# Optimization experiments

Hardware: AMD Instinct MI355X
Metric: run time of the kernel (lower is better)

## Reference

```python
import jax, jax.numpy as jnp
import numpy as np

B, S, D, H = 2, 2048, 1024, 16
Dh = D // H
LN_EPS = 1e-5


def setup_inputs() -> dict:
    key = jax.random.key(0)
    ks = jax.random.split(key, 14)
    s = 1.0 / np.sqrt(D)
    return {
        "q": jax.random.normal(ks[0], (B, S, D), jnp.float32),
        "k": jax.random.normal(ks[1], (B, S, D), jnp.float32),
        "v": jax.random.normal(ks[2], (B, S, D), jnp.float32),
        "attn_mask": jax.random.randint(ks[3], (B, S, S), 0, 2).astype(bool),
        "Wq": jax.random.normal(ks[4], (D, D), jnp.float32) * s,
        "bq": jnp.zeros((D,), jnp.float32),
        "Wk": jax.random.normal(ks[5], (D, D), jnp.float32) * s,
        "bk": jnp.zeros((D,), jnp.float32),
        "Wv": jax.random.normal(ks[6], (D, D), jnp.float32) * s,
        "bv": jnp.zeros((D,), jnp.float32),
        "Wo": jax.random.normal(ks[7], (D, D), jnp.float32) * s,
        "bo": jnp.zeros((D,), jnp.float32),
        "gamma": jnp.ones((D,), jnp.float32),
        "beta": jnp.zeros((D,), jnp.float32),
    }


def reference(q, k, v, attn_mask, Wq, bq, Wk, bk, Wv, bv, Wo, bo, gamma, beta):
    residual = q
    # projections (W stored as [in, out])
    qh = (q @ Wq + bq).reshape(B, S, H, Dh).transpose(0, 2, 1, 3)  # [B,H,S,Dh]
    kh = (k @ Wk + bk).reshape(B, S, H, Dh).transpose(0, 2, 1, 3)
    vh = (v @ Wv + bv).reshape(B, S, H, Dh).transpose(0, 2, 1, 3)
    scores = jnp.einsum("bhqd,bhkd->bhqk", qh, kh) / np.sqrt(Dh)
    scores = jnp.where(attn_mask[:, None, :, :], -1e9, scores)
    attn = jax.nn.softmax(scores, axis=-1)  # dropout is identity in eval
    context = jnp.einsum("bhqk,bhkd->bhqd", attn, vh)  # [B,H,S,Dh]
    # faithful to original bug: flat reshape WITHOUT transposing heads back
    context = context.reshape(B, S, D)
    out = context @ Wo + bo
    x = residual + out
    mu = jnp.mean(x, axis=-1, keepdims=True)
    var = jnp.var(x, axis=-1, keepdims=True)
    out = (x - mu) / jnp.sqrt(var + LN_EPS) * gamma + beta
    return out, attn
```

## Files before the change

### kernel.cpp

```cpp
#include <hip/hip_runtime.h>
#include <hip/hip_bf16.h>

typedef __attribute__((ext_vector_type(8))) short bf16x8;
typedef __attribute__((ext_vector_type(4))) float f32x4;

__device__ __forceinline__ short f2bf(float f) {
    union { float f; unsigned u; } v; v.f = f;
    unsigned r = (v.u + 0x7FFFu + ((v.u >> 16) & 1u)) >> 16;
    return (short)r;
}
__device__ __forceinline__ float bf2f(short s) {
    union { unsigned u; float f; } v; v.u = ((unsigned)(unsigned short)s) << 16;
    return v.f;
}
__device__ __forceinline__ void gll16(const void* g, void* l) {
    __builtin_amdgcn_global_load_lds(
        (const __attribute__((address_space(1))) unsigned int*)g,
        (__attribute__((address_space(3))) unsigned int*)l, 16, 0, 0);
}

#define QSCALE 0.18033688011112042f

__global__ __launch_bounds__(256) void k_prep(
    const float* __restrict__ qin, const float* __restrict__ kin, const float* __restrict__ vin,
    short* __restrict__ qbf, short* __restrict__ kbf, short* __restrict__ vbf,
    const float* __restrict__ Wq, const float* __restrict__ Wk,
    const float* __restrict__ Wv, const float* __restrict__ Wo,
    short* __restrict__ WqT, short* __restrict__ WkT,
    short* __restrict__ WvT, short* __restrict__ WoT,
    const int* __restrict__ mask, unsigned* __restrict__ mb)
{
    __shared__ int sm[8192];
    const int bid = blockIdx.x, tid = threadIdx.x;
    if (bid < 6144) {
        const float* in = bid < 2048 ? qin : (bid < 4096 ? kin : vin);
        short* out = bid < 2048 ? qbf : (bid < 4096 ? kbf : vbf);
        const long i = ((long)(bid & 2047) * 256 + tid) * 8;
        float4 f0 = *reinterpret_cast<const float4*>(&in[i]);
        float4 f1 = *reinterpret_cast<const float4*>(&in[i + 4]);
        bf16x8 v;
        v[0] = f2bf(f0.x); v[1] = f2bf(f0.y); v[2] = f2bf(f0.z); v[3] = f2bf(f0.w);
        v[4] = f2bf(f1.x); v[5] = f2bf(f1.y); v[6] = f2bf(f1.z); v[7] = f2bf(f1.w);
        *reinterpret_cast<bf16x8*>(&out[i]) = v;
    } else if (bid < 10240) {
        const int t2 = bid - 6144, which = t2 >> 10, local = t2 & 1023;
        const float* W = which == 0 ? Wq : (which == 1 ? Wk : (which == 2 ? Wv : Wo));
        short* WT = which == 0 ? WqT : (which == 1 ? WkT : (which == 2 ? WvT : WoT));
        float (*t)[33] = reinterpret_cast<float(*)[33]>(sm);
        const int rb = (local >> 5) * 32, cb = (local & 31) * 32;
        const int tr = tid >> 3, tc = (tid & 7) * 4;
        const float4 v = *reinterpret_cast<const float4*>(&W[(long)(rb + tr) * 1024 + cb + tc]);
        t[tr][tc + 0] = v.x; t[tr][tc + 1] = v.y; t[tr][tc + 2] = v.z; t[tr][tc + 3] = v.w;
        __syncthreads();
        short4 o;
        o.x = f2bf(t[tc + 0][tr]); o.y = f2bf(t[tc + 1][tr]);
        o.z = f2bf(t[tc + 2][tr]); o.w = f2bf(t[tc + 3][tr]);
        *reinterpret_cast<short4*>(&WT[(long)(cb + tr) * 1024 + rb + tc]) = o;
    } else {
        const long base = (long)(bid - 10240) * 8192;
#pragma unroll
        for (int i = 0; i < 8; ++i)
            *reinterpret_cast<int4*>(&sm[i * 1024 + tid * 4]) =
                *reinterpret_cast<const int4*>(&mask[base + i * 1024 + tid * 4]);
        __syncthreads();
        unsigned wv = 0;
#pragma unroll
        for (int j = 0; j < 32; ++j) wv |= (sm[tid * 32 + j] != 0 ? 1u : 0u) << j;
        mb[base / 32 + tid] = wv;
    }
}

__global__ __launch_bounds__(256) void k_gemm_qkv(
    const short* __restrict__ A0, const short* __restrict__ A1, const short* __restrict__ A2,
    const short* __restrict__ B0, const short* __restrict__ B1, const short* __restrict__ B2,
    const float* __restrict__ b0, const float* __restrict__ b1, const float* __restrict__ b2,
    short* __restrict__ o0, short* __restrict__ o1, short* __restrict__ o2)
{
    __shared__ short As[128 * 64];
    __shared__ short Bs[128 * 64];
    const int z = blockIdx.z;
    const short* A = z == 0 ? A0 : (z == 1 ? A1 : A2);
    const short* BT = z == 0 ? B0 : (z == 1 ? B1 : B2);
    const float* bias = z == 0 ? b0 : (z == 1 ? b1 : b2);
    short* outp = z == 0 ? o0 : (z == 1 ? o1 : o2);
    const float scale = z == 0 ? QSCALE : 1.0f;

    const int tid = threadIdx.x, w = tid >> 6, lane = tid & 63;
    const int lr = lane & 15, lg = lane >> 4;
    const int rowbase = blockIdx.y * 128, colbase = blockIdx.x * 128;
    const int wr = (w >> 1) * 64, wc = (w & 1) * 64;
    const int srow = lane >> 3, sc_ = (lane & 7) ^ srow;

    f32x4 acc[4][4] = {};

    for (int kb = 0; kb < 1024; kb += 64) {
#pragma unroll
        for (int ii = 0; ii < 4; ++ii) {
            const int rl = w * 32 + ii * 8 + srow;
            gll16(A + (long)(rowbase + rl) * 1024 + kb + sc_ * 8, &As[(w * 32 + ii * 8) * 64]);
            gll16(BT + (long)(colbase + rl) * 1024 + kb + sc_ * 8, &Bs[(w * 32 + ii * 8) * 64]);
        }
        __syncthreads();
#pragma unroll
        for (int ks = 0; ks < 2; ++ks) {
            bf16x8 a[4], bq[4];
#pragma unroll
            for (int m = 0; m < 4; ++m) {
                const int r = wr + m * 16 + lr;
                a[m] = *reinterpret_cast<const bf16x8*>(&As[r * 64 + (((ks * 4 + lg) ^ (r & 7)) << 3)]);
            }
#pragma unroll
            for (int n = 0; n < 4; ++n) {
                const int r = wc + n * 16 + lr;
                bq[n] = *reinterpret_cast<const bf16x8*>(&Bs[r * 64 + (((ks * 4 + lg) ^ (r & 7)) << 3)]);
            }
#pragma unroll
            for (int m = 0; m < 4; ++m)
#pragma unroll
                for (int n = 0; n < 4; ++n)
                    acc[m][n] = __builtin_amdgcn_mfma_f32_16x16x32_bf16(a[m], bq[n], acc[m][n], 0, 0, 0);
        }
        __syncthreads();
    }

#pragma unroll
    for (int m = 0; m < 4; ++m) {
#pragma unroll
        for (int n = 0; n < 4; ++n) {
            const int C = colbase + wc + n * 16 + lr;
            const float bv = bias[C];
#pragma unroll
            for (int rr = 0; rr < 4; ++rr) {
                const int R = rowbase + wr + m * 16 + lg * 4 + rr;
                const float val = (acc[m][n][rr] + bv) * scale;
                const int b = R >> 11, s = R & 2047, h = C >> 6, dh = C & 63;
                if (z != 2)
                    outp[(((long)(b * 16 + h) * 2048 + s) << 6) + dh] = f2bf(val);
                else
                    outp[(((long)(b * 16 + h) * 64 + dh) << 11) + s] = f2bf(val);
            }
        }
    }
}

__global__ __launch_bounds__(256) void k_gemm_o(
    const short* __restrict__ A, const short* __restrict__ BT,
    const float* __restrict__ bias, const float* __restrict__ resid,
    float* __restrict__ outp)
{
    __shared__ short As[128 * 64];
    __shared__ short Bs[128 * 64];
    const int tid = threadIdx.x, w = tid >> 6, lane = tid & 63;
    const int lr = lane & 15, lg = lane >> 4;
    const int rowbase = blockIdx.y * 128, colbase = blockIdx.x * 128;
    const int wr = (w >> 1) * 64, wc = (w & 1) * 64;
    const int srow = lane >> 3, sc_ = (lane & 7) ^ srow;

    f32x4 acc[4][4] = {};

    for (int kb = 0; kb < 1024; kb += 64) {
#pragma unroll
        for (int ii = 0; ii < 4; ++ii) {
            const int rl = w * 32 + ii * 8 + srow;
            gll16(A + (long)(rowbase + rl) * 1024 + kb + sc_ * 8, &As[(w * 32 + ii * 8) * 64]);
            gll16(BT + (long)(colbase + rl) * 1024 + kb + sc_ * 8, &Bs[(w * 32 + ii * 8) * 64]);
        }
        __syncthreads();
#pragma unroll
        for (int ks = 0; ks < 2; ++ks) {
            bf16x8 a[4], bq[4];
#pragma unroll
            for (int m = 0; m < 4; ++m) {
                const int r = wr + m * 16 + lr;
                a[m] = *reinterpret_cast<const bf16x8*>(&As[r * 64 + (((ks * 4 + lg) ^ (r & 7)) << 3)]);
            }
#pragma unroll
            for (int n = 0; n < 4; ++n) {
                const int r = wc + n * 16 + lr;
                bq[n] = *reinterpret_cast<const bf16x8*>(&Bs[r * 64 + (((ks * 4 + lg) ^ (r & 7)) << 3)]);
            }
#pragma unroll
            for (int m = 0; m < 4; ++m)
#pragma unroll
                for (int n = 0; n < 4; ++n)
                    acc[m][n] = __builtin_amdgcn_mfma_f32_16x16x32_bf16(a[m], bq[n], acc[m][n], 0, 0, 0);
        }
        __syncthreads();
    }

#pragma unroll
    for (int m = 0; m < 4; ++m) {
#pragma unroll
        for (int n = 0; n < 4; ++n) {
            const int C = colbase + wc + n * 16 + lr;
            const float bv = bias[C];
#pragma unroll
            for (int rr = 0; rr < 4; ++rr) {
                const int R = rowbase + wr + m * 16 + lg * 4 + rr;
                const long idx = (long)R * 1024 + C;
                outp[idx] = acc[m][n][rr] + bv + resid[idx];
            }
        }
    }
}

__global__ __launch_bounds__(256, 4) void k_attn(
    const short* __restrict__ qh, const short* __restrict__ kh,
    const short* __restrict__ vt, const unsigned* __restrict__ mbits,
    float* __restrict__ attn_out, short* __restrict__ ctxb)
{
    const int g = blockIdx.x, xcd = g & 7, u = g >> 3;
    const int bh = u >> 2, qt = xcd * 4 + (u & 3);
    const int b = bh >> 4;
    const int tid = threadIdx.x, w = tid >> 6, lane = tid & 63;
    const int lr = lane & 15, lg = lane >> 4;
    const int irow = qt * 64 + w * 16;
    const long arow = (long)bh * 2048 + irow;

    __shared__ short Ks[2][64 * 64];
    __shared__ short Vs[2][64 * 64];
    __shared__ short Ps[4][16 * 64];

    const short* qhp = qh + arow * 64;
    const short* khp = kh + (long)bh * 131072;
    const short* vtp = vt + (long)bh * 131072;
    const unsigned* mbp = mbits + (long)b * 131072 + (long)irow * 64;

    const bf16x8 aq0 = *reinterpret_cast<const bf16x8*>(&qhp[lr * 64 + lg * 8]);
    const bf16x8 aq1 = *reinterpret_cast<const bf16x8*>(&qhp[lr * 64 + 32 + lg * 8]);
    const int srow = lane >> 3, sc_ = (lane & 7) ^ srow;

    auto stage_k = [&](int buf, int ch) {
#pragma unroll
        for (int ii = 0; ii < 2; ++ii) {
            const int r0 = w * 16 + ii * 8;
            gll16(khp + (long)(ch * 64 + r0 + srow) * 64 + sc_ * 8, &Ks[buf][r0 * 64]);
        }
    };
    auto stage_v = [&](int buf, int ch) {
#pragma unroll
        for (int ii = 0; ii < 2; ++ii) {
            const int r0 = w * 16 + ii * 8;
            gll16(vtp + (long)(r0 + srow) * 2048 + ch * 64 + sc_ * 8, &Vs[buf][r0 * 64]);
        }
    };
    auto kfrag = [&](int buf, int t, int ks) -> bf16x8 {
        const int r = t * 16 + lr;
        return *reinterpret_cast<const bf16x8*>(&Ks[buf][r * 64 + (((ks * 4 + lg) ^ (r & 7)) << 3)]);
    };
    auto vfrag = [&](int buf, int gi, int ks) -> bf16x8 {
        const int r = gi * 16 + lr;
        return *reinterpret_cast<const bf16x8*>(&Vs[buf][r * 64 + (((ks * 4 + lg) ^ (r & 7)) << 3)]);
    };
    auto ps_write = [&](int row, int t, float p) {
        const int ch8 = (t * 2 + (lr >> 3)) ^ (row & 7);
        Ps[w][row * 64 + (ch8 << 3) + (lr & 7)] = f2bf(p);
    };

    float l[4] = {0.f, 0.f, 0.f, 0.f};
    f32x4 acc[4] = {};

    stage_k(0, 0); stage_v(0, 0);
    asm volatile("s_waitcnt vmcnt(0)" ::: "memory");
    __builtin_amdgcn_s_barrier();
    asm volatile("" ::: "memory");

    for (int ch = 0; ch < 32; ++ch) {
        const int cur = ch & 1;
        unsigned mw[4][2];
#pragma unroll
        for (int rr = 0; rr < 4; ++rr) {
            mw[rr][0] = mbp[(lg * 4 + rr) * 64 + ch * 2];
            mw[rr][1] = mbp[(lg * 4 + rr) * 64 + ch * 2 + 1];
        }
        asm volatile("" ::: "memory");
        if (ch < 31) { stage_k(cur ^ 1, ch + 1); stage_v(cur ^ 1, ch + 1); }
        asm volatile("" ::: "memory");

#pragma unroll
        for (int t = 0; t < 4; ++t) {
            f32x4 sc = {};
            sc = __builtin_amdgcn_mfma_f32_16x16x32_bf16(aq0, kfrag(cur, t, 0), sc, 0, 0, 0);
            sc = __builtin_amdgcn_mfma_f32_16x16x32_bf16(aq1, kfrag(cur, t, 1), sc, 0, 0, 0);
#pragma unroll
            for (int rr = 0; rr < 4; ++rr) {
                const bool masked = (mw[rr][t >> 1] >> (((t & 1) << 4) + lr)) & 1;
                const float p = exp2f(masked ? -1e9f : sc[rr]);
                l[rr] += p;
                ps_write(lg * 4 + rr, t, p);
            }
        }
        const bf16x8 pa0 = *reinterpret_cast<const bf16x8*>(&Ps[w][lr * 64 + (((0 * 4 + lg) ^ (lr & 7)) << 3)]);
        const bf16x8 pa1 = *reinterpret_cast<const bf16x8*>(&Ps[w][lr * 64 + (((1 * 4 + lg) ^ (lr & 7)) << 3)]);
#pragma unroll
        for (int gi = 0; gi < 4; ++gi) {
            acc[gi] = __builtin_amdgcn_mfma_f32_16x16x32_bf16(pa0, vfrag(cur, gi, 0), acc[gi], 0, 0, 0);
            acc[gi] = __builtin_amdgcn_mfma_f32_16x16x32_bf16(pa1, vfrag(cur, gi, 1), acc[gi], 0, 0, 0);
        }
        asm volatile("s_waitcnt vmcnt(0)" ::: "memory");
        __builtin_amdgcn_s_barrier();
        asm volatile("" ::: "memory");
    }

    float C[4];
#pragma unroll
    for (int rr = 0; rr < 4; ++rr) {
#pragma unroll
        for (int off = 1; off < 16; off <<= 1) l[rr] += __shfl_xor(l[rr], off, 16);
        l[rr] = fmaxf(l[rr], 1e-30f);
        C[rr] = log2f(l[rr]);
    }
#pragma unroll
    for (int gi = 0; gi < 4; ++gi)
#pragma unroll
        for (int rr = 0; rr < 4; ++rr)
            ctxb[(arow + lg * 4 + rr) * 64 + gi * 16 + lr] = f2bf(acc[gi][rr] / l[rr]);

    stage_k(0, 0);
    asm volatile("s_waitcnt vmcnt(0)" ::: "memory");
    __builtin_amdgcn_s_barrier();
    asm volatile("" ::: "memory");

    for (int ch = 0; ch < 32; ++ch) {
        const int cur = ch & 1;
        unsigned mw[4][2];
#pragma unroll
        for (int rr = 0; rr < 4; ++rr) {
            mw[rr][0] = mbp[(lg * 4 + rr) * 64 + ch * 2];
            mw[rr][1] = mbp[(lg * 4 + rr) * 64 + ch * 2 + 1];
        }
        asm volatile("" ::: "memory");
        if (ch < 31) stage_k(cur ^ 1, ch + 1);
        asm volatile("" ::: "memory");

#pragma unroll
        for (int t = 0; t < 4; ++t) {
            f32x4 sc = {};
            sc = __builtin_amdgcn_mfma_f32_16x16x32_bf16(aq0, kfrag(cur, t, 0), sc, 0, 0, 0);
            sc = __builtin_amdgcn_mfma_f32_16x16x32_bf16(aq1, kfrag(cur, t, 1), sc, 0, 0, 0);
#pragma unroll
            for (int rr = 0; rr < 4; ++rr) {
                const bool masked = (mw[rr][t >> 1] >> (((t & 1) << 4) + lr)) & 1;
                const float p = exp2f((masked ? -1e9f : sc[rr]) - C[rr]);
                ps_write(lg * 4 + rr, t, p);
            }
        }
#pragma unroll
        for (int i2 = 0; i2 < 4; ++i2) {
            const int r = i2 * 4 + lg;
            const short4 p4 = *reinterpret_cast<const short4*>(
                &Ps[w][r * 64 + ((((lr >> 1)) ^ (r & 7)) << 3) + ((lr & 1) << 2)]);
            float4 o;
            o.x = bf2f(p4.x); o.y = bf2f(p4.y); o.z = bf2f(p4.z); o.w = bf2f(p4.w);
            *reinterpret_cast<float4*>(&attn_out[(arow + r) * 2048 + ch * 64 + lr * 4]) = o;
        }
        asm volatile("s_waitcnt vmcnt(4)" ::: "memory");
        __builtin_amdgcn_s_barrier();
        asm volatile("" ::: "memory");
    }
}

__global__ __launch_bounds__(256) void k_ln(const float* __restrict__ x,
    const float* __restrict__ gamma, const float* __restrict__ beta,
    float* __restrict__ out)
{
    __shared__ float red[8];
    const int r = blockIdx.x, tid = threadIdx.x;
    const float4 v = reinterpret_cast<const float4*>(x + (long)r * 1024)[tid];
    float s = v.x + v.y + v.z + v.w;
    float q2 = v.x * v.x + v.y * v.y + v.z * v.z + v.w * v.w;
#pragma unroll
    for (int off = 32; off; off >>= 1) {
        s += __shfl_xor(s, off, 64);
        q2 += __shfl_xor(q2, off, 64);
    }
    if ((tid & 63) == 0) { red[(tid >> 6) * 2] = s; red[(tid >> 6) * 2 + 1] = q2; }
    __syncthreads();
    s = red[0] + red[2] + red[4] + red[6];
    q2 = red[1] + red[3] + red[5] + red[7];
    const float mu = s * (1.0f / 1024.0f);
    const float var = q2 * (1.0f / 1024.0f) - mu * mu;
    const float rs = rsqrtf(var + 1e-5f);
    const float4 gm = reinterpret_cast<const float4*>(gamma)[tid];
    const float4 bb = reinterpret_cast<const float4*>(beta)[tid];
    float4 o;
    o.x = (v.x - mu) * rs * gm.x + bb.x;
    o.y = (v.y - mu) * rs * gm.y + bb.y;
    o.z = (v.z - mu) * rs * gm.z + bb.z;
    o.w = (v.w - mu) * rs * gm.w + bb.w;
    reinterpret_cast<float4*>(out + (long)r * 1024)[tid] = o;
}

extern "C" void kernel_launch(void* const* d_in, const int* in_sizes, int n_in,
                              void* d_out, int out_size, void* d_ws, size_t ws_size,
                              hipStream_t stream)
{
    const float* qin  = (const float*)d_in[0];
    const float* kin  = (const float*)d_in[1];
    const float* vin  = (const float*)d_in[2];
    const int*   mask = (const int*)d_in[3];
    const float* Wq = (const float*)d_in[4];
    const float* bq = (const float*)d_in[5];
    const float* Wk = (const float*)d_in[6];
    const float* bk = (const float*)d_in[7];
    const float* Wv = (const float*)d_in[8];
    const float* bv = (const float*)d_in[9];
    const float* Wo = (const float*)d_in[10];
    const float* bo = (const float*)d_in[11];
    const float* gamma = (const float*)d_in[12];
    const float* beta  = (const float*)d_in[13];

    char* ws = (char*)d_ws;
    short* WqT = (short*)(ws + (0ul  << 20));
    short* WkT = (short*)(ws + (2ul  << 20));
    short* WvT = (short*)(ws + (4ul  << 20));
    short* WoT = (short*)(ws + (6ul  << 20));
    short* qbf = (short*)(ws + (8ul  << 20));
    short* kbf = (short*)(ws + (16ul << 20));
    short* vbf = (short*)(ws + (24ul << 20));
    short* qh  = (short*)(ws + (32ul << 20));
    short* khb = (short*)(ws + (40ul << 20));
    short* vtb = (short*)(ws + (48ul << 20));
    unsigned* mb = (unsigned*)(ws + (56ul << 20));
    short* ctxb = (short*)(ws + (57ul << 20));
    float* xb   = (float*)(ws + (8ul  << 20));

    float* outLN = (float*)d_out;
    float* attnO = (float*)d_out + 4194304;

    const dim3 blk(256);
    k_prep<<<dim3(11264), blk, 0, stream>>>(qin, kin, vin, qbf, kbf, vbf,
                                            Wq, Wk, Wv, Wo, WqT, WkT, WvT, WoT, mask, mb);
    k_gemm_qkv<<<dim3(8, 32, 3), blk, 0, stream>>>(qbf, kbf, vbf, WqT, WkT, WvT,
                                                   bq, bk, bv, qh, khb, vtb);
    k_attn<<<dim3(1024), blk, 0, stream>>>(qh, khb, vtb, mb, attnO, ctxb);
    k_gemm_o<<<dim3(8, 32), blk, 0, stream>>>(ctxb, WoT, bo, qin, xb);
    k_ln<<<dim3(4096), blk, 0, stream>>>(xb, gamma, beta, outLN);
}
```

Before: 336.1 us.

## Unify K/V LDS buffers and process two attention chunks per barrier in pass two

The second attention pass (probability emission) now reuses a four-slot LDS array for K, processing two 64-key chunks per iteration with prefetch two chunks ahead, which halves the number of barriers and deepens the load pipeline. Separately, the V-transpose projection epilogue writes four consecutive bf16 values as one short4 store instead of four scalar stores. The V path also drops the scale multiply, which is presumably 1 for V. The risks are extra in-flight loads and register pressure from holding two mask sets, plus a wrap-around prefetch of chunks 0 and 1 at the end.

```diff
diff --git a/kernel.cpp b/kernel.cpp
--- a/kernel.cpp
+++ b/kernel.cpp
@@ -129,15 +129,23 @@
         for (int n = 0; n < 4; ++n) {
             const int C = colbase + wc + n * 16 + lr;
             const float bv = bias[C];
-#pragma unroll
-            for (int rr = 0; rr < 4; ++rr) {
-                const int R = rowbase + wr + m * 16 + lg * 4 + rr;
-                const float val = (acc[m][n][rr] + bv) * scale;
-                const int b = R >> 11, s = R & 2047, h = C >> 6, dh = C & 63;
-                if (z != 2)
+            if (z != 2) {
+#pragma unroll
+                for (int rr = 0; rr < 4; ++rr) {
+                    const int R = rowbase + wr + m * 16 + lg * 4 + rr;
+                    const float val = (acc[m][n][rr] + bv) * scale;
+                    const int b = R >> 11, s = R & 2047, h = C >> 6, dh = C & 63;
                     outp[(((long)(b * 16 + h) * 2048 + s) << 6) + dh] = f2bf(val);
-                else
-                    outp[(((long)(b * 16 + h) * 64 + dh) << 11) + s] = f2bf(val);
+                }
+            } else {
+                const int R0 = rowbase + wr + m * 16 + lg * 4;
+                const int b = R0 >> 11, s0 = R0 & 2047, h = C >> 6, dh = C & 63;
+                short4 o;
+                o.x = f2bf(acc[m][n][0] + bv);
+                o.y = f2bf(acc[m][n][1] + bv);
+                o.z = f2bf(acc[m][n][2] + bv);
+                o.w = f2bf(acc[m][n][3] + bv);
+                *reinterpret_cast<short4*>(&outp[(((long)(b * 16 + h) * 64 + dh) << 11) + s0]) = o;
             }
         }
     }
@@ -217,8 +225,7 @@
     const int irow = qt * 64 + w * 16;
     const long arow = (long)bh * 2048 + irow;
 
-    __shared__ short Ks[2][64 * 64];
-    __shared__ short Vs[2][64 * 64];
+    __shared__ short KV[4][64 * 64];
     __shared__ short Ps[4][16 * 64];
 
     const short* qhp = qh + arow * 64;
@@ -234,23 +241,23 @@
 #pragma unroll
         for (int ii = 0; ii < 2; ++ii) {
             const int r0 = w * 16 + ii * 8;
-            gll16(khp + (long)(ch * 64 + r0 + srow) * 64 + sc_ * 8, &Ks[buf][r0 * 64]);
+            gll16(khp + (long)(ch * 64 + r0 + srow) * 64 + sc_ * 8, &KV[buf][r0 * 64]);
         }
     };
     auto stage_v = [&](int buf, int ch) {
 #pragma unroll
         for (int ii = 0; ii < 2; ++ii) {
             const int r0 = w * 16 + ii * 8;
-            gll16(vtp + (long)(r0 + srow) * 2048 + ch * 64 + sc_ * 8, &Vs[buf][r0 * 64]);
+            gll16(vtp + (long)(r0 + srow) * 2048 + ch * 64 + sc_ * 8, &KV[2 + buf][r0 * 64]);
         }
     };
     auto kfrag = [&](int buf, int t, int ks) -> bf16x8 {
         const int r = t * 16 + lr;
-        return *reinterpret_cast<const bf16x8*>(&Ks[buf][r * 64 + (((ks * 4 + lg) ^ (r & 7)) << 3)]);
+        return *reinterpret_cast<const bf16x8*>(&KV[buf][r * 64 + (((ks * 4 + lg) ^ (r & 7)) << 3)]);
     };
     auto vfrag = [&](int buf, int gi, int ks) -> bf16x8 {
         const int r = gi * 16 + lr;
-        return *reinterpret_cast<const bf16x8*>(&Vs[buf][r * 64 + (((ks * 4 + lg) ^ (r & 7)) << 3)]);
+        return *reinterpret_cast<const bf16x8*>(&KV[2 + buf][r * 64 + (((ks * 4 + lg) ^ (r & 7)) << 3)]);
     };
     auto ps_write = [&](int row, int t, float p) {
         const int ch8 = (t * 2 + (lr >> 3)) ^ (row & 7);
@@ -316,28 +323,13 @@
         for (int rr = 0; rr < 4; ++rr)
             ctxb[(arow + lg * 4 + rr) * 64 + gi * 16 + lr] = f2bf(acc[gi][rr] / l[rr]);
 
-    stage_k(0, 0);
-    asm volatile("s_waitcnt vmcnt(0)" ::: "memory");
-    __builtin_amdgcn_s_barrier();
-    asm volatile("" ::: "memory");
-
-    for (int ch = 0; ch < 32; ++ch) {
-        const int cur = ch & 1;
-        unsigned mw[4][2];
-#pragma unroll
-        for (int rr = 0; rr < 4; ++rr) {
-            mw[rr][0] = mbp[(lg * 4 + rr) * 64 + ch * 2];
-            mw[rr][1] = mbp[(lg * 4 + rr) * 64 + ch * 2 + 1];
-        }
-        asm volatile("" ::: "memory");
-        if (ch < 31) stage_k(cur ^ 1, ch + 1);
-        asm volatile("" ::: "memory");
-
+    auto emit_chunk = [&](int ch, unsigned (&mw)[4][2]) {
+        const int buf = ch & 3;
 #pragma unroll
         for (int t = 0; t < 4; ++t) {
             f32x4 sc = {};
-            sc = __builtin_amdgcn_mfma_f32_16x16x32_bf16(aq0, kfrag(cur, t, 0), sc, 0, 0, 0);
-            sc = __builtin_amdgcn_mfma_f32_16x16x32_bf16(aq1, kfrag(cur, t, 1), sc, 0, 0, 0);
+            sc = __builtin_amdgcn_mfma_f32_16x16x32_bf16(aq0, kfrag(buf, t, 0), sc, 0, 0, 0);
+            sc = __builtin_amdgcn_mfma_f32_16x16x32_bf16(aq1, kfrag(buf, t, 1), sc, 0, 0, 0);
 #pragma unroll
             for (int rr = 0; rr < 4; ++rr) {
                 const bool masked = (mw[rr][t >> 1] >> (((t & 1) << 4) + lr)) & 1;
@@ -354,7 +346,32 @@
             o.x = bf2f(p4.x); o.y = bf2f(p4.y); o.z = bf2f(p4.z); o.w = bf2f(p4.w);
             *reinterpret_cast<float4*>(&attn_out[(arow + r) * 2048 + ch * 64 + lr * 4]) = o;
         }
-        asm volatile("s_waitcnt vmcnt(4)" ::: "memory");
+    };
+
+    stage_k(0, 0); stage_k(1, 1);
+    asm volatile("s_waitcnt vmcnt(0)" ::: "memory");
+    __builtin_amdgcn_s_barrier();
+    asm volatile("" ::: "memory");
+
+    for (int it = 0; it < 16; ++it) {
+        const int chA = it * 2, chB = chA + 1;
+        unsigned mwA[4][2], mwB[4][2];
+#pragma unroll
+        for (int rr = 0; rr < 4; ++rr) {
+            mwA[rr][0] = mbp[(lg * 4 + rr) * 64 + chA * 2];
+            mwA[rr][1] = mbp[(lg * 4 + rr) * 64 + chA * 2 + 1];
+            mwB[rr][0] = mbp[(lg * 4 + rr) * 64 + chB * 2];
+            mwB[rr][1] = mbp[(lg * 4 + rr) * 64 + chB * 2 + 1];
+        }
+        asm volatile("" ::: "memory");
+        stage_k((chA + 2) & 3, (chA + 2) & 31);
+        stage_k((chB + 2) & 3, (chB + 2) & 31);
+        asm volatile("" ::: "memory");
+
+        emit_chunk(chA, mwA);
+        emit_chunk(chB, mwB);
+
+        asm volatile("s_waitcnt vmcnt(8)" ::: "memory");
         __builtin_amdgcn_s_barrier();
         asm volatile("" ::: "memory");
     }
```

After: 312.8 us. -6.9%, faster.
